# Performance work log

Hardware: AMD Instinct MI355X
Metric: run time of the kernel (lower is better)

Reference implementation:

```python
import jax, jax.numpy as jnp
import numpy as np

H = 1.0  # primo_h
N_GRID = 768


def _grid_mesh(n):
    ii, jj = np.meshgrid(np.arange(n - 1), np.arange(n - 1), indexing='ij')
    v00 = (ii * n + jj).ravel(); v10 = ((ii + 1) * n + jj).ravel()
    v01 = (ii * n + jj + 1).ravel(); v11 = ((ii + 1) * n + jj + 1).ravel()
    tri1 = np.stack([v00, v10, v01], 1); tri2 = np.stack([v10, v11, v01], 1)
    return np.concatenate([tri1, tri2], 0).astype(np.int32)  # [F,3]


def _face_adjacency(faces):
    # faces: [F,3] -> edges [E,2] (sorted vertex pairs), face_ids [E,2]
    F = faces.shape[0]
    fe = np.stack([faces[:, [0, 1]], faces[:, [1, 2]], faces[:, [2, 0]]], 1).reshape(-1, 2)
    fe = np.sort(fe, axis=1)
    fid = np.repeat(np.arange(F, dtype=np.int32), 3)
    order = np.lexsort((fe[:, 1], fe[:, 0]))
    fs, fi = fe[order], fid[order]
    same = np.all(fs[:-1] == fs[1:], axis=1)
    k = np.nonzero(same)[0]
    edges = fs[k].astype(np.int32)
    face_ids = np.stack([fi[k], fi[k + 1]], 1).astype(np.int32)
    return edges, face_ids


def setup_inputs() -> dict:
    key = jax.random.key(0)
    k1, k2, k3 = jax.random.split(key, 3)
    faces_np = _grid_mesh(N_GRID)                      # [F,3]
    edges_np, face_ids_np = _face_adjacency(faces_np)  # [E,2],[E,2]
    F = faces_np.shape[0]
    V = N_GRID * N_GRID
    return {
        'transformed_prism': jax.random.normal(k1, (F, 3, 3), dtype=jnp.float32),
        'rotations': jax.random.normal(k2, (F, 3, 3), dtype=jnp.float32),
        'verts': jax.random.normal(k3, (1, V, 3), dtype=jnp.float32),
        'faces': jnp.asarray(faces_np.T),       # [3,F], matches torch forward arg
        'edges': jnp.asarray(edges_np),
        'face_ids': jnp.asarray(face_ids_np),
    }


def _verts_id_face(Ft, E, Q):
    # Ft: [F,3] faces; E: [e,2] edge vertex ids; Q: [e,2] adjacent face ids
    fa, fb = Ft[Q[:, 0]], Ft[Q[:, 1]]  # [e,3]

    def find(fv, tgt):
        return jnp.where(fv[:, 0] == tgt, 0,
               jnp.where(fv[:, 1] == tgt, 1,
               jnp.where(fv[:, 2] == tgt, 2, -1)))

    return jnp.stack([find(fa, E[:, 0]), find(fa, E[:, 1]),
                      find(fb, E[:, 0]), find(fb, E[:, 1])], axis=1)  # [e,4]


def reference(transformed_prism, rotations, verts, faces, edges, face_ids):
    tp = transformed_prism
    bs = verts.shape[0]
    v = verts.reshape(-1, 3)
    Ft = faces.T  # [F,3]

    # per-face normals (vectorized version of the original per-face loop)
    e1 = tp[:, 0] - tp[:, 1]
    e2 = tp[:, 0] - tp[:, 2]
    nrm = jnp.cross(e1, e2)
    normals = nrm / jnp.linalg.norm(nrm, axis=-1, keepdims=True)  # [F,3]

    # face areas
    p1, p2, p3 = v[Ft[:, 0]], v[Ft[:, 1]], v[Ft[:, 2]]
    face_areas = 0.5 * jnp.linalg.norm(jnp.cross(p2 - p1, p3 - p1), axis=1)

    # faithful to original: normals indexed by edge VERTEX ids
    n1, n2 = normals[edges[:, 0]], normals[edges[:, 1]]
    fid1, fid2 = face_ids[:, 0], face_ids[:, 1]
    r1, r2 = rotations[fid1], rotations[fid2]

    ftv = _verts_id_face(Ft, edges, face_ids)  # [e,4]
    v1_p1, v2_p1 = tp[fid1, ftv[:, 0]], tp[fid1, ftv[:, 1]]
    v1_p2, v2_p2 = tp[fid2, ftv[:, 2]], tp[fid2, ftv[:, 3]]

    p1n1 = jnp.einsum('ec,ecd->ed', n1, r1)
    p1n2 = jnp.einsum('ec,ecd->ed', n2, r1)
    p2n1 = jnp.einsum('ec,ecd->ed', n1, r2)
    p2n2 = jnp.einsum('ec,ecd->ed', n2, r2)

    A = jnp.stack([v1_p1 + p1n1 * H, v2_p1 + p1n2 * H,
                   v1_p1 - p1n1 * H, v2_p1 - p1n2 * H], axis=1)  # [e,4,3]
    B = jnp.stack([v1_p2 + p2n1 * H, v2_p2 + p2n2 * H,
                   v1_p2 - p2n1 * H, v2_p2 - p2n2 * H], axis=1)
    D = A - B

    # coeff[p,q] = 2^{-|i_p-i_q|-|j_p-j_q|}, (i,j) over {0,1}^2
    idx = jnp.array([[0, 0], [0, 1], [1, 0], [1, 1]], dtype=jnp.float32)
    coeff = 2.0 ** (-jnp.abs(idx[:, None] - idx[None, :]).sum(-1))  # [4,4]
    pair = jnp.einsum('epc,eqc->epq', D, D)
    energy = (pair * coeff).sum((1, 2)) / 9.0  # [e]

    weight = jnp.sum((v[edges[:, 0]] - v[edges[:, 1]]) ** 2, axis=1) \
             / (face_areas[fid1] + face_areas[fid2])
    return (energy * weight).sum() / bs
```

## Files before the change

### kernel.cpp

```cpp
#include <hip/hip_runtime.h>


#define BI 8
#define BJ 8
#define T2ROW 84
#define VROW  28
#define NSTRIDE 28
#define T2_CH 189
#define V_CH  70
#define NORM_CNT 81

struct __attribute__((aligned(4))) F4s { float a, b, c, d; };
struct F3 { float x, y, z; };
struct R9 { float v[9]; };

__device__ __forceinline__ R9 load9(const float* __restrict__ p) {
    R9 r;
    F4s u0 = *(const F4s*)p;
    F4s u1 = *(const F4s*)(p + 4);
    r.v[0] = u0.a; r.v[1] = u0.b; r.v[2] = u0.c; r.v[3] = u0.d;
    r.v[4] = u1.a; r.v[5] = u1.b; r.v[6] = u1.c; r.v[7] = u1.d;
    r.v[8] = p[8];
    return r;
}

__device__ __forceinline__ int imin(int a, int b) { return a < b ? a : b; }
__device__ __forceinline__ int imax(int a, int b) { return a > b ? a : b; }

__device__ __forceinline__ void gload_lds16(const float* gp, float* lp) {
    __builtin_amdgcn_global_load_lds(
        (const __attribute__((address_space(1))) void*)gp,
        (__attribute__((address_space(3))) void*)lp, 16, 0, 0);
}

__device__ __forceinline__ F3 normal_of(const R9& r) {
    float e1x = r.v[0] - r.v[3], e1y = r.v[1] - r.v[4], e1z = r.v[2] - r.v[5];
    float e2x = r.v[0] - r.v[6], e2y = r.v[1] - r.v[7], e2z = r.v[2] - r.v[8];
    float nx = e1y * e2z - e1z * e2y;
    float ny = e1z * e2x - e1x * e2z;
    float nz = e1x * e2y - e1y * e2x;
    float inv = 1.0f / sqrtf(nx * nx + ny * ny + nz * nz);
    F3 o; o.x = nx * inv; o.y = ny * inv; o.z = nz * inv; return o;
}

__device__ __forceinline__ float tri_area_p(const float* p, const float* q,
                                            const float* r) {
    float ax = q[0] - p[0], ay = q[1] - p[1], az = q[2] - p[2];
    float bx = r[0] - p[0], by = r[1] - p[1], bz = r[2] - p[2];
    float cx = ay * bz - az * by, cy = az * bx - ax * bz, cz = ax * by - ay * bx;
    return 0.5f * sqrtf(cx * cx + cy * cy + cz * cz);
}

__device__ __forceinline__ float edge_ew(const float* u1, const float* u2,
                                         const float* w1, const float* w2,
                                         const float* rA, const float* rB,
                                         const F3& n1, const F3& n2,
                                         const float* pa, const float* pb,
                                         float asum) {
    float ux = u1[0] - u2[0], uy = u1[1] - u2[1], uz = u1[2] - u2[2];
    float wx = w1[0] - w2[0], wy = w1[1] - w2[1], wz = w1[2] - w2[2];

    float d0 = rA[0] - rB[0], d1 = rA[1] - rB[1], d2 = rA[2] - rB[2];
    float d3 = rA[3] - rB[3], d4 = rA[4] - rB[4], d5 = rA[5] - rB[5];
    float d6 = rA[6] - rB[6], d7 = rA[7] - rB[7], d8 = rA[8] - rB[8];

    float ax = n1.x * d0 + n1.y * d3 + n1.z * d6;
    float ay = n1.x * d1 + n1.y * d4 + n1.z * d7;
    float az = n1.x * d2 + n1.y * d5 + n1.z * d8;
    float bx = n2.x * d0 + n2.y * d3 + n2.z * d6;
    float by = n2.x * d1 + n2.y * d4 + n2.z * d7;
    float bz = n2.x * d2 + n2.y * d5 + n2.z * d8;

    float uu = ux * ux + uy * uy + uz * uz;
    float ww = wx * wx + wy * wy + wz * wz;
    float uw = ux * wx + uy * wy + uz * wz;
    float aa = ax * ax + ay * ay + az * az;
    float bb = bx * bx + by * by + bz * bz;
    float ab = ax * bx + ay * by + az * bz;
    float energy = (3.0f * (uu + ww + uw) + (aa + bb + ab)) * (1.0f / 9.0f);

    float dx = pa[0] - pb[0], dy = pa[1] - pb[1], dz = pa[2] - pb[2];
    return energy * (dx * dx + dy * dy + dz * dz) / asum;
}

__global__ __launch_bounds__(64) void fused_kernel(
        const float* __restrict__ tp,
        const float* __restrict__ rot,
        const float* __restrict__ verts,
        double* __restrict__ partials,
        int n) {
    const int m = n - 1;
    const int Q = m * m;
    const int F = 2 * Q;
    const int V = n * n;
    const int lane = threadIdx.x;
    const int i0 = blockIdx.y * BI;
    const int j0 = blockIdx.x * BJ;
    const int w = lane >> 3;
    const int l = lane & 7;
    const int i = i0 + w;
    const int j = j0 + l;

    __shared__ __attribute__((aligned(16))) float sT2[9 * T2ROW];
    __shared__ __attribute__((aligned(16))) float sR2[9 * T2ROW];
    __shared__ __attribute__((aligned(16))) float sV[10 * VROW];
    __shared__ float sVh[10 * 4];
    __shared__ float sN[9 * NSTRIDE];

    int f1 = imin(i, m - 1) * m + imin(j, m - 1);
    R9 t1 = load9(tp  + (size_t)9 * f1);
    R9 r1 = load9(rot + (size_t)9 * f1);

#pragma unroll
    for (int it = 0; it < 8; ++it) {
        if (it < 6) {
            int a = it >= 3;
            int ch = (a ? it - 3 : it) * 64 + lane;
            if (ch < T2_CH) {
                int r = ch / 21, c = ch - 21 * r;
                int gi = imin(i0 - 1 + r, m - 1);
                int g = 9 * (Q + gi * m + (j0 - 1)) + 4 * c;
                g = imin(g, 9 * F - 4);
                gload_lds16((a ? rot : tp) + g,
                            (a ? sR2 : sT2) + ch * 4);
            }
        } else {
            int ch = (it - 6) * 64 + lane;
            if (ch < V_CH) {
                int r = ch / 7, c = ch - 7 * r;
                int vr = imax(imin(i0 - 1 + r, n - 1), 0);
                int g = 3 * (vr * n + j0) + 4 * c;
                g = imin(g, 3 * V - 4);
                gload_lds16(verts + g, sV + ch * 4);
            }
        }
    }

    float hval = 0.0f;
    float* hdst = nullptr;
    if (lane < 30) {
        int r = lane / 3, k = lane - 3 * r;
        int vr = imax(imin(i0 - 1 + r, n - 1), 0);
        int g = imax(3 * (vr * n + (j0 - 1)) + k, 0);
        hval = verts[g];
        hdst = sVh + r * 4 + k;
    }

    R9 nraw[2];
    int nofs[2];
#pragma unroll
    for (int it = 0; it < 2; ++it) {
        int s = lane + 64 * it;
        bool act = s < NORM_CNT;
        int sc = act ? s : 0;
        int r = sc / 9, c = sc - 9 * r;
        int gi = imin(i0 + r, n - 1);
        int gj = imin(j0 + c, n - 1);
        nraw[it] = load9(tp + (size_t)9 * (gi * n + gj));
        nofs[it] = act ? (r * NSTRIDE + 3 * c) : -1;
    }

    if (hdst) *hdst = hval;
#pragma unroll
    for (int it = 0; it < 2; ++it) {
        if (nofs[it] >= 0) {
            F3 nm = normal_of(nraw[it]);
            sN[nofs[it]] = nm.x; sN[nofs[it] + 1] = nm.y; sN[nofs[it] + 2] = nm.z;
        }
    }

    __syncthreads();

    double term = 0.0;
    if (i < m && j < m) {
        const float* t2c = sT2 + (w + 1) * T2ROW + 9 * (l + 1);
        const float* r2c = sR2 + (w + 1) * T2ROW + 9 * (l + 1);
        const float* th  = sT2 + w * T2ROW + 9 * (l + 1);
        const float* rh  = sR2 + w * T2ROW + 9 * (l + 1);
        const float* tv  = sT2 + (w + 1) * T2ROW + 9 * l;
        const float* rv  = sR2 + (w + 1) * T2ROW + 9 * l;

        const float* p00 = sV + (w + 1) * VROW + 3 * l;
        const float* p01 = p00 + 3;
        const float* p10 = sV + (w + 2) * VROW + 3 * l;
        const float* p11 = p10 + 3;
        const float* pup = sV + w * VROW + 3 * (l + 1);
        const float* plf = l ? sV + (w + 2) * VROW + 3 * (l - 1)
                             : sVh + (w + 2) * 4;

        const float* na = sN + w * NSTRIDE + 3 * l;
        const float* nb = na + 3;
        const float* nc = sN + (w + 1) * NSTRIDE + 3 * l;
        F3 nA = { na[0], na[1], na[2] };
        F3 nB = { nb[0], nb[1], nb[2] };
        F3 nC = { nc[0], nc[1], nc[2] };

        float a1   = tri_area_p(p00, p10, p01);
        float a2c  = tri_area_p(p10, p11, p01);
        float a2up = tri_area_p(p00, p01, pup);
        float a2lf = tri_area_p(plf, p10, p00);

        float sum = edge_ew(t1.v + 6, t2c + 6, t1.v + 3, t2c + 0, r1.v, r2c,
                            nB, nC, p01, p10, a1 + a2c);
        float eh = edge_ew(t1.v + 0, th + 0, t1.v + 6, th + 3, r1.v, rh,
                           nA, nB, p00, p01, a1 + a2up);
        float ev = edge_ew(t1.v + 0, tv + 6, t1.v + 3, tv + 3, r1.v, rv,
                           nA, nC, p00, p10, a1 + a2lf);
        sum += (i > 0 ? eh : 0.0f);
        sum += (j > 0 ? ev : 0.0f);
        term = (double)sum;
    }

#pragma unroll
    for (int off = 32; off > 0; off >>= 1) term += __shfl_down(term, off, 64);
    if (lane == 0)
        partials[blockIdx.y * gridDim.x + blockIdx.x] = term;
}

__global__ __launch_bounds__(256) void finalize_kernel(
        const double* __restrict__ partials, int P, float* __restrict__ out) {
    double s = 0.0;
    for (int i = threadIdx.x; i < P; i += 256) s += partials[i];
#pragma unroll
    for (int off = 32; off > 0; off >>= 1) s += __shfl_down(s, off, 64);
    __shared__ double sred[4];
    int lane = threadIdx.x & 63, wid = threadIdx.x >> 6;
    if (lane == 0) sred[wid] = s;
    __syncthreads();
    if (threadIdx.x == 0) out[0] = (float)(sred[0] + sred[1] + sred[2] + sred[3]);
}

extern "C" void kernel_launch(void* const* d_in, const int* in_sizes, int n_in,
                              void* d_out, int out_size, void* d_ws, size_t ws_size,
                              hipStream_t stream) {
    const float* tp    = (const float*)d_in[0];
    const float* rot   = (const float*)d_in[1];
    const float* verts = (const float*)d_in[2];

    int V = in_sizes[2] / 3;
    int n = (int)(sqrtf((float)V) + 0.5f);
    int m = n - 1;

    double* partials = (double*)d_ws;
    float*  out      = (float*)d_out;

    dim3 grid((m + BJ - 1) / BJ, (m + BI - 1) / BI);
    int P = grid.x * grid.y;
    fused_kernel<<<grid, 64, 0, stream>>>(tp, rot, verts, partials, n);
    finalize_kernel<<<1, 256, 0, stream>>>(partials, P, out);
}
```

Measured before the change: 159.5 us.

## Widen tile to 8x16 cells per block with two cells per thread and block swizzle

```diff
diff --git a/kernel.cpp b/kernel.cpp
--- a/kernel.cpp
+++ b/kernel.cpp
@@ -2,13 +2,13 @@
 
 
 #define BI 8
-#define BJ 8
-#define T2ROW 84
-#define VROW  28
-#define NSTRIDE 28
-#define T2_CH 189
-#define V_CH  70
-#define NORM_CNT 81
+#define BJ 16
+#define FST 156
+#define FSLOTS 351
+#define VST 52
+#define VSLOTS 130
+#define NST 52
+#define NCNT 153
 
 struct __attribute__((aligned(4))) F4s { float a, b, c, d; };
 struct F3 { float x, y, z; };
@@ -94,45 +94,55 @@
     const int F = 2 * Q;
     const int V = n * n;
     const int lane = threadIdx.x;
-    const int i0 = blockIdx.y * BI;
-    const int j0 = blockIdx.x * BJ;
+
+    const int gx = gridDim.x;
+    const int nb = gx * gridDim.y;
+    const int b  = blockIdx.y * gx + blockIdx.x;
+    const int b2 = (nb & 7) ? b : ((b & 7) * (nb >> 3) + (b >> 3));
+    const int by = b2 / gx;
+    const int bx = b2 - by * gx;
+    const int i0 = by * BI;
+    const int j0 = bx * BJ;
+
     const int w = lane >> 3;
     const int l = lane & 7;
     const int i = i0 + w;
-    const int j = j0 + l;
-
-    __shared__ __attribute__((aligned(16))) float sT2[9 * T2ROW];
-    __shared__ __attribute__((aligned(16))) float sR2[9 * T2ROW];
-    __shared__ __attribute__((aligned(16))) float sV[10 * VROW];
+
+    __shared__ __attribute__((aligned(16))) float sT2[9 * FST];
+    __shared__ __attribute__((aligned(16))) float sR2[9 * FST];
+    __shared__ __attribute__((aligned(16))) float sV[10 * VST];
     __shared__ float sVh[10 * 4];
-    __shared__ float sN[9 * NSTRIDE];
-
-    int f1 = imin(i, m - 1) * m + imin(j, m - 1);
-    R9 t1 = load9(tp  + (size_t)9 * f1);
-    R9 r1 = load9(rot + (size_t)9 * f1);
-
-#pragma unroll
-    for (int it = 0; it < 8; ++it) {
-        if (it < 6) {
-            int a = it >= 3;
-            int ch = (a ? it - 3 : it) * 64 + lane;
-            if (ch < T2_CH) {
-                int r = ch / 21, c = ch - 21 * r;
-                int gi = imin(i0 - 1 + r, m - 1);
-                int g = 9 * (Q + gi * m + (j0 - 1)) + 4 * c;
-                g = imin(g, 9 * F - 4);
-                gload_lds16((a ? rot : tp) + g,
-                            (a ? sR2 : sT2) + ch * 4);
-            }
-        } else {
-            int ch = (it - 6) * 64 + lane;
-            if (ch < V_CH) {
-                int r = ch / 7, c = ch - 7 * r;
-                int vr = imax(imin(i0 - 1 + r, n - 1), 0);
-                int g = 3 * (vr * n + j0) + 4 * c;
-                g = imin(g, 3 * V - 4);
-                gload_lds16(verts + g, sV + ch * 4);
-            }
+    __shared__ float sN[9 * NST];
+
+    int iq  = imin(i, m - 1);
+    int f1a = iq * m + imin(j0 + l, m - 1);
+    int f1b = iq * m + imin(j0 + l + 8, m - 1);
+    R9 t1a = load9(tp  + (size_t)9 * f1a);
+    R9 r1a = load9(rot + (size_t)9 * f1a);
+    R9 t1b = load9(tp  + (size_t)9 * f1b);
+    R9 r1b = load9(rot + (size_t)9 * f1b);
+
+#pragma unroll
+    for (int it = 0; it < 12; ++it) {
+        int a = it >= 6;
+        int ch = (a ? it - 6 : it) * 64 + lane;
+        if (ch < FSLOTS) {
+            int r = ch / 39, c = ch - 39 * r;
+            int gi = imin(i0 - 1 + r, m - 1);
+            int g = 9 * (Q + gi * m + (j0 - 1)) + 4 * c;
+            g = imin(g, 9 * F - 4);
+            gload_lds16((a ? rot : tp) + g, (a ? sR2 : sT2) + ch * 4);
+        }
+    }
+#pragma unroll
+    for (int it = 0; it < 3; ++it) {
+        int ch = it * 64 + lane;
+        if (ch < VSLOTS) {
+            int r = ch / 13, c = ch - 13 * r;
+            int vr = imax(imin(i0 - 1 + r, n - 1), 0);
+            int g = 3 * (vr * n + j0) + 4 * c;
+            g = imin(g, 3 * V - 4);
+            gload_lds16(verts + g, sV + ch * 4);
         }
     }
 
@@ -146,23 +156,23 @@
         hdst = sVh + r * 4 + k;
     }
 
-    R9 nraw[2];
-    int nofs[2];
-#pragma unroll
-    for (int it = 0; it < 2; ++it) {
+    R9 nraw[3];
+    int nofs[3];
+#pragma unroll
+    for (int it = 0; it < 3; ++it) {
         int s = lane + 64 * it;
-        bool act = s < NORM_CNT;
+        bool act = s < NCNT;
         int sc = act ? s : 0;
-        int r = sc / 9, c = sc - 9 * r;
+        int r = sc / 17, c = sc - 17 * r;
         int gi = imin(i0 + r, n - 1);
         int gj = imin(j0 + c, n - 1);
         nraw[it] = load9(tp + (size_t)9 * (gi * n + gj));
-        nofs[it] = act ? (r * NSTRIDE + 3 * c) : -1;
+        nofs[it] = act ? (r * NST + 3 * c) : -1;
     }
 
     if (hdst) *hdst = hval;
 #pragma unroll
-    for (int it = 0; it < 2; ++it) {
+    for (int it = 0; it < 3; ++it) {
         if (nofs[it] >= 0) {
             F3 nm = normal_of(nraw[it]);
             sN[nofs[it]] = nm.x; sN[nofs[it] + 1] = nm.y; sN[nofs[it] + 2] = nm.z;
@@ -172,43 +182,53 @@
     __syncthreads();
 
     double term = 0.0;
-    if (i < m && j < m) {
-        const float* t2c = sT2 + (w + 1) * T2ROW + 9 * (l + 1);
-        const float* r2c = sR2 + (w + 1) * T2ROW + 9 * (l + 1);
-        const float* th  = sT2 + w * T2ROW + 9 * (l + 1);
-        const float* rh  = sR2 + w * T2ROW + 9 * (l + 1);
-        const float* tv  = sT2 + (w + 1) * T2ROW + 9 * l;
-        const float* rv  = sR2 + (w + 1) * T2ROW + 9 * l;
-
-        const float* p00 = sV + (w + 1) * VROW + 3 * l;
-        const float* p01 = p00 + 3;
-        const float* p10 = sV + (w + 2) * VROW + 3 * l;
-        const float* p11 = p10 + 3;
-        const float* pup = sV + w * VROW + 3 * (l + 1);
-        const float* plf = l ? sV + (w + 2) * VROW + 3 * (l - 1)
-                             : sVh + (w + 2) * 4;
-
-        const float* na = sN + w * NSTRIDE + 3 * l;
-        const float* nb = na + 3;
-        const float* nc = sN + (w + 1) * NSTRIDE + 3 * l;
-        F3 nA = { na[0], na[1], na[2] };
-        F3 nB = { nb[0], nb[1], nb[2] };
-        F3 nC = { nc[0], nc[1], nc[2] };
-
-        float a1   = tri_area_p(p00, p10, p01);
-        float a2c  = tri_area_p(p10, p11, p01);
-        float a2up = tri_area_p(p00, p01, pup);
-        float a2lf = tri_area_p(plf, p10, p00);
-
-        float sum = edge_ew(t1.v + 6, t2c + 6, t1.v + 3, t2c + 0, r1.v, r2c,
-                            nB, nC, p01, p10, a1 + a2c);
-        float eh = edge_ew(t1.v + 0, th + 0, t1.v + 6, th + 3, r1.v, rh,
-                           nA, nB, p00, p01, a1 + a2up);
-        float ev = edge_ew(t1.v + 0, tv + 6, t1.v + 3, tv + 3, r1.v, rv,
-                           nA, nC, p00, p10, a1 + a2lf);
-        sum += (i > 0 ? eh : 0.0f);
-        sum += (j > 0 ? ev : 0.0f);
-        term = (double)sum;
+    if (i < m) {
+#pragma unroll
+        for (int q = 0; q < 2; ++q) {
+            const int lq = l + 8 * q;
+            const int jq = j0 + lq;
+            if (jq < m) {
+                const R9& t1 = q ? t1b : t1a;
+                const R9& r1 = q ? r1b : r1a;
+
+                const float* t2c = sT2 + (w + 1) * FST + 9 * (lq + 1);
+                const float* r2c = sR2 + (w + 1) * FST + 9 * (lq + 1);
+                const float* th  = sT2 + w * FST + 9 * (lq + 1);
+                const float* rh  = sR2 + w * FST + 9 * (lq + 1);
+                const float* tv  = sT2 + (w + 1) * FST + 9 * lq;
+                const float* rv  = sR2 + (w + 1) * FST + 9 * lq;
+
+                const float* p00 = sV + (w + 1) * VST + 3 * lq;
+                const float* p01 = p00 + 3;
+                const float* p10 = sV + (w + 2) * VST + 3 * lq;
+                const float* p11 = p10 + 3;
+                const float* pup = sV + w * VST + 3 * (lq + 1);
+                const float* plf = lq ? sV + (w + 2) * VST + 3 * (lq - 1)
+                                      : sVh + (w + 2) * 4;
+
+                const float* na = sN + w * NST + 3 * lq;
+                const float* nb = na + 3;
+                const float* nc = sN + (w + 1) * NST + 3 * lq;
+                F3 nA = { na[0], na[1], na[2] };
+                F3 nB = { nb[0], nb[1], nb[2] };
+                F3 nC = { nc[0], nc[1], nc[2] };
+
+                float a1   = tri_area_p(p00, p10, p01);
+                float a2c  = tri_area_p(p10, p11, p01);
+                float a2up = tri_area_p(p00, p01, pup);
+                float a2lf = tri_area_p(plf, p10, p00);
+
+                float sum = edge_ew(t1.v + 6, t2c + 6, t1.v + 3, t2c + 0,
+                                    r1.v, r2c, nB, nC, p01, p10, a1 + a2c);
+                float eh = edge_ew(t1.v + 0, th + 0, t1.v + 6, th + 3,
+                                   r1.v, rh, nA, nB, p00, p01, a1 + a2up);
+                float ev = edge_ew(t1.v + 0, tv + 6, t1.v + 3, tv + 3,
+                                   r1.v, rv, nA, nC, p00, p10, a1 + a2lf);
+                sum += (i > 0 ? eh : 0.0f);
+                sum += (jq > 0 ? ev : 0.0f);
+                term += (double)sum;
+            }
+        }
     }
 
 #pragma unroll
```

After: 155.9 us. 2.3% less time.

## Replace LDS-staged 8x8 tiles with direct per-thread global loads in 64x4 blocks

Applied to the files above, without the earlier changes.

```diff
diff --git a/kernel.cpp b/kernel.cpp
--- a/kernel.cpp
+++ b/kernel.cpp
@@ -1,14 +1,5 @@
 #include <hip/hip_runtime.h>
 
-
-#define BI 8
-#define BJ 8
-#define T2ROW 84
-#define VROW  28
-#define NSTRIDE 28
-#define T2_CH 189
-#define V_CH  70
-#define NORM_CNT 81
 
 struct __attribute__((aligned(4))) F4s { float a, b, c, d; };
 struct F3 { float x, y, z; };
@@ -24,14 +15,12 @@
     return r;
 }
 
+__device__ __forceinline__ F3 loadv3(const float* __restrict__ p) {
+    F3 r; r.x = p[0]; r.y = p[1]; r.z = p[2]; return r;
+}
+
 __device__ __forceinline__ int imin(int a, int b) { return a < b ? a : b; }
 __device__ __forceinline__ int imax(int a, int b) { return a > b ? a : b; }
-
-__device__ __forceinline__ void gload_lds16(const float* gp, float* lp) {
-    __builtin_amdgcn_global_load_lds(
-        (const __attribute__((address_space(1))) void*)gp,
-        (__attribute__((address_space(3))) void*)lp, 16, 0, 0);
-}
 
 __device__ __forceinline__ F3 normal_of(const R9& r) {
     float e1x = r.v[0] - r.v[3], e1y = r.v[1] - r.v[4], e1z = r.v[2] - r.v[5];
@@ -43,10 +32,9 @@
     F3 o; o.x = nx * inv; o.y = ny * inv; o.z = nz * inv; return o;
 }
 
-__device__ __forceinline__ float tri_area_p(const float* p, const float* q,
-                                            const float* r) {
-    float ax = q[0] - p[0], ay = q[1] - p[1], az = q[2] - p[2];
-    float bx = r[0] - p[0], by = r[1] - p[1], bz = r[2] - p[2];
+__device__ __forceinline__ float tri_area(const F3& p, const F3& q, const F3& r) {
+    float ax = q.x - p.x, ay = q.y - p.y, az = q.z - p.z;
+    float bx = r.x - p.x, by = r.y - p.y, bz = r.z - p.z;
     float cx = ay * bz - az * by, cy = az * bx - ax * bz, cz = ax * by - ay * bx;
     return 0.5f * sqrtf(cx * cx + cy * cy + cz * cz);
 }
@@ -55,7 +43,7 @@
                                          const float* w1, const float* w2,
                                          const float* rA, const float* rB,
                                          const F3& n1, const F3& n2,
-                                         const float* pa, const float* pb,
+                                         const F3& pa, const F3& pb,
                                          float asum) {
     float ux = u1[0] - u2[0], uy = u1[1] - u2[1], uz = u1[2] - u2[2];
     float wx = w1[0] - w2[0], wy = w1[1] - w2[1], wz = w1[2] - w2[2];
@@ -79,11 +67,11 @@
     float ab = ax * bx + ay * by + az * bz;
     float energy = (3.0f * (uu + ww + uw) + (aa + bb + ab)) * (1.0f / 9.0f);
 
-    float dx = pa[0] - pb[0], dy = pa[1] - pb[1], dz = pa[2] - pb[2];
+    float dx = pa.x - pb.x, dy = pa.y - pb.y, dz = pa.z - pb.z;
     return energy * (dx * dx + dy * dy + dz * dz) / asum;
 }
 
-__global__ __launch_bounds__(64) void fused_kernel(
+__global__ __launch_bounds__(256) void fused_kernel(
         const float* __restrict__ tp,
         const float* __restrict__ rot,
         const float* __restrict__ verts,
@@ -91,130 +79,66 @@
         int n) {
     const int m = n - 1;
     const int Q = m * m;
-    const int F = 2 * Q;
-    const int V = n * n;
-    const int lane = threadIdx.x;
-    const int i0 = blockIdx.y * BI;
-    const int j0 = blockIdx.x * BJ;
-    const int w = lane >> 3;
-    const int l = lane & 7;
-    const int i = i0 + w;
-    const int j = j0 + l;
+    const int tid = threadIdx.x;
+    const int lane = tid & 63;
+    const int wv = tid >> 6;
+    const int i = blockIdx.y * 4 + wv;
+    const int j = blockIdx.x * 64 + lane;
+    const bool act = (i < m) && (j < m);
 
-    __shared__ __attribute__((aligned(16))) float sT2[9 * T2ROW];
-    __shared__ __attribute__((aligned(16))) float sR2[9 * T2ROW];
-    __shared__ __attribute__((aligned(16))) float sV[10 * VROW];
-    __shared__ float sVh[10 * 4];
-    __shared__ float sN[9 * NSTRIDE];
+    const int ic = imin(i, m - 1);
+    const int jc = imin(j, m - 1);
 
-    int f1 = imin(i, m - 1) * m + imin(j, m - 1);
-    R9 t1 = load9(tp  + (size_t)9 * f1);
-    R9 r1 = load9(rot + (size_t)9 * f1);
+    const int f1 = ic * m + jc;
+    const int fd = Q + f1;
+    const int fh = Q + imax(ic - 1, 0) * m + jc;
+    const int fv = Q + ic * m + imax(jc - 1, 0);
 
-#pragma unroll
-    for (int it = 0; it < 8; ++it) {
-        if (it < 6) {
-            int a = it >= 3;
-            int ch = (a ? it - 3 : it) * 64 + lane;
-            if (ch < T2_CH) {
-                int r = ch / 21, c = ch - 21 * r;
-                int gi = imin(i0 - 1 + r, m - 1);
-                int g = 9 * (Q + gi * m + (j0 - 1)) + 4 * c;
-                g = imin(g, 9 * F - 4);
-                gload_lds16((a ? rot : tp) + g,
-                            (a ? sR2 : sT2) + ch * 4);
-            }
-        } else {
-            int ch = (it - 6) * 64 + lane;
-            if (ch < V_CH) {
-                int r = ch / 7, c = ch - 7 * r;
-                int vr = imax(imin(i0 - 1 + r, n - 1), 0);
-                int g = 3 * (vr * n + j0) + 4 * c;
-                g = imin(g, 3 * V - 4);
-                gload_lds16(verts + g, sV + ch * 4);
-            }
-        }
-    }
+    R9 t1  = load9(tp  + (size_t)9 * f1);
+    R9 r1  = load9(rot + (size_t)9 * f1);
+    R9 t2  = load9(tp  + (size_t)9 * fd);
+    R9 r2  = load9(rot + (size_t)9 * fd);
+    R9 thh = load9(tp  + (size_t)9 * fh);
+    R9 rhh = load9(rot + (size_t)9 * fh);
+    R9 tvv = load9(tp  + (size_t)9 * fv);
+    R9 rvv = load9(rot + (size_t)9 * fv);
 
-    float hval = 0.0f;
-    float* hdst = nullptr;
-    if (lane < 30) {
-        int r = lane / 3, k = lane - 3 * r;
-        int vr = imax(imin(i0 - 1 + r, n - 1), 0);
-        int g = imax(3 * (vr * n + (j0 - 1)) + k, 0);
-        hval = verts[g];
-        hdst = sVh + r * 4 + k;
-    }
+    const int v00 = ic * n + jc;
+    F3 p00 = loadv3(verts + (size_t)3 * v00);
+    F3 p01 = loadv3(verts + (size_t)3 * (v00 + 1));
+    F3 p10 = loadv3(verts + (size_t)3 * (v00 + n));
+    F3 p11 = loadv3(verts + (size_t)3 * (v00 + n + 1));
+    F3 pup = loadv3(verts + (size_t)3 * (imax(ic - 1, 0) * n + jc + 1));
+    F3 plf = loadv3(verts + (size_t)3 * (v00 + n - 1));
 
-    R9 nraw[2];
-    int nofs[2];
-#pragma unroll
-    for (int it = 0; it < 2; ++it) {
-        int s = lane + 64 * it;
-        bool act = s < NORM_CNT;
-        int sc = act ? s : 0;
-        int r = sc / 9, c = sc - 9 * r;
-        int gi = imin(i0 + r, n - 1);
-        int gj = imin(j0 + c, n - 1);
-        nraw[it] = load9(tp + (size_t)9 * (gi * n + gj));
-        nofs[it] = act ? (r * NSTRIDE + 3 * c) : -1;
-    }
+    F3 nA = normal_of(load9(tp + (size_t)9 * (size_t)(ic * n + jc)));
+    F3 nB = normal_of(load9(tp + (size_t)9 * (size_t)(ic * n + jc + 1)));
+    F3 nC = normal_of(load9(tp + (size_t)9 * (size_t)((ic + 1) * n + jc)));
 
-    if (hdst) *hdst = hval;
-#pragma unroll
-    for (int it = 0; it < 2; ++it) {
-        if (nofs[it] >= 0) {
-            F3 nm = normal_of(nraw[it]);
-            sN[nofs[it]] = nm.x; sN[nofs[it] + 1] = nm.y; sN[nofs[it] + 2] = nm.z;
-        }
-    }
+    float a1   = tri_area(p00, p10, p01);
+    float a2c  = tri_area(p10, p11, p01);
+    float a2up = tri_area(p00, p01, pup);
+    float a2lf = tri_area(plf, p10, p00);
 
-    __syncthreads();
+    float sum = edge_ew(t1.v + 6, t2.v + 6, t1.v + 3, t2.v + 0, r1.v, r2.v,
+                        nB, nC, p01, p10, a1 + a2c);
+    float eh = edge_ew(t1.v + 0, thh.v + 0, t1.v + 6, thh.v + 3, r1.v, rhh.v,
+                       nA, nB, p00, p01, a1 + a2up);
+    float ev = edge_ew(t1.v + 0, tvv.v + 6, t1.v + 3, tvv.v + 3, r1.v, rvv.v,
+                       nA, nC, p00, p10, a1 + a2lf);
+    sum += (i > 0 ? eh : 0.0f);
+    sum += (j > 0 ? ev : 0.0f);
 
-    double term = 0.0;
-    if (i < m && j < m) {
-        const float* t2c = sT2 + (w + 1) * T2ROW + 9 * (l + 1);
-        const float* r2c = sR2 + (w + 1) * T2ROW + 9 * (l + 1);
-        const float* th  = sT2 + w * T2ROW + 9 * (l + 1);
-        const float* rh  = sR2 + w * T2ROW + 9 * (l + 1);
-        const float* tv  = sT2 + (w + 1) * T2ROW + 9 * l;
-        const float* rv  = sR2 + (w + 1) * T2ROW + 9 * l;
+    double term = act ? (double)sum : 0.0;
 
-        const float* p00 = sV + (w + 1) * VROW + 3 * l;
-        const float* p01 = p00 + 3;
-        const float* p10 = sV + (w + 2) * VROW + 3 * l;
-        const float* p11 = p10 + 3;
-        const float* pup = sV + w * VROW + 3 * (l + 1);
-        const float* plf = l ? sV + (w + 2) * VROW + 3 * (l - 1)
-                             : sVh + (w + 2) * 4;
-
-        const float* na = sN + w * NSTRIDE + 3 * l;
-        const float* nb = na + 3;
-        const float* nc = sN + (w + 1) * NSTRIDE + 3 * l;
-        F3 nA = { na[0], na[1], na[2] };
-        F3 nB = { nb[0], nb[1], nb[2] };
-        F3 nC = { nc[0], nc[1], nc[2] };
-
-        float a1   = tri_area_p(p00, p10, p01);
-        float a2c  = tri_area_p(p10, p11, p01);
-        float a2up = tri_area_p(p00, p01, pup);
-        float a2lf = tri_area_p(plf, p10, p00);
-
-        float sum = edge_ew(t1.v + 6, t2c + 6, t1.v + 3, t2c + 0, r1.v, r2c,
-                            nB, nC, p01, p10, a1 + a2c);
-        float eh = edge_ew(t1.v + 0, th + 0, t1.v + 6, th + 3, r1.v, rh,
-                           nA, nB, p00, p01, a1 + a2up);
-        float ev = edge_ew(t1.v + 0, tv + 6, t1.v + 3, tv + 3, r1.v, rv,
-                           nA, nC, p00, p10, a1 + a2lf);
-        sum += (i > 0 ? eh : 0.0f);
-        sum += (j > 0 ? ev : 0.0f);
-        term = (double)sum;
-    }
-
+    __shared__ double sred[4];
 #pragma unroll
     for (int off = 32; off > 0; off >>= 1) term += __shfl_down(term, off, 64);
-    if (lane == 0)
-        partials[blockIdx.y * gridDim.x + blockIdx.x] = term;
+    if (lane == 0) sred[wv] = term;
+    __syncthreads();
+    if (tid == 0)
+        partials[blockIdx.y * gridDim.x + blockIdx.x] =
+            sred[0] + sred[1] + sred[2] + sred[3];
 }
 
 __global__ __launch_bounds__(256) void finalize_kernel(
@@ -244,8 +168,8 @@
     double* partials = (double*)d_ws;
     float*  out      = (float*)d_out;
 
-    dim3 grid((m + BJ - 1) / BJ, (m + BI - 1) / BI);
+    dim3 grid((m + 63) / 64, (m + 3) / 4);
     int P = grid.x * grid.y;
-    fused_kernel<<<grid, 64, 0, stream>>>(tp, rot, verts, partials, n);
+    fused_kernel<<<grid, 256, 0, stream>>>(tp, rot, verts, partials, n);
     finalize_kernel<<<1, 256, 0, stream>>>(partials, P, out);
 }
```

Result: no change. 161.2 us (+1.0%).
